# Performance work log

Measured on AMD Instinct MI355X. Metric: run time of the kernel, lower is better.

The kernel has to match this reference:

```python
import jax, jax.numpy as jnp
import numpy as np

N_GRAPHS = 256      # graphs in the batch
N_PER = 52          # nodes per peptide graph (module default num_nodes=52)
IN_CH = 21          # amino-acid one-hot features
HIDDEN = 128
OUT_EG = 128
LATENT = 64
N_LAYERS = 4


def _fc_edges(n_graphs, n_per):
    """Block-diagonal fully-connected directed edges (no self loops)."""
    base = np.arange(n_per)
    r, c = np.meshgrid(base, base, indexing='ij')
    mask = r != c
    r, c = r[mask], c[mask]                       # [n_per*(n_per-1)]
    offs = (np.arange(n_graphs) * n_per)[:, None]
    row = (r[None, :] + offs).reshape(-1)
    col = (c[None, :] + offs).reshape(-1)
    return row.astype(np.int32), col.astype(np.int32)


def setup_inputs() -> dict:
    key = jax.random.key(0)
    ks = iter(jax.random.split(key, 40))

    def rn(shape, scale=0.05):
        return jax.random.normal(next(ks), shape, dtype=jnp.float32) * scale

    N = N_GRAPHS * N_PER
    row, col = _fc_edges(N_GRAPHS, N_PER)
    L, H = N_LAYERS, HIDDEN
    return {
        'x': jax.random.normal(next(ks), (N, IN_CH), dtype=jnp.float32),
        'pos': jax.random.normal(next(ks), (N, 3), dtype=jnp.float32),
        'edge_row': jnp.asarray(row),
        'edge_col': jnp.asarray(col),
        'batch': jnp.repeat(jnp.arange(N_GRAPHS, dtype=jnp.int32), N_PER),
        'emb_in_w': rn((IN_CH, H)), 'emb_in_b': jnp.zeros((H,), jnp.float32),
        'edge_w1': rn((L, 2 * H + 1, H)), 'edge_b1': jnp.zeros((L, H), jnp.float32),
        'edge_w2': rn((L, H, H)), 'edge_b2': jnp.zeros((L, H), jnp.float32),
        'node_w1': rn((L, 2 * H, H)), 'node_b1': jnp.zeros((L, H), jnp.float32),
        'node_w2': rn((L, H, H)), 'node_b2': jnp.zeros((L, H), jnp.float32),
        'coord_w1': rn((L, H, H)), 'coord_b1': jnp.zeros((L, H), jnp.float32),
        'coord_w2': rn((L, H, 1), scale=0.001),   # xavier gain=0.001, no bias
        'emb_out_w': rn((H, OUT_EG)), 'emb_out_b': jnp.zeros((OUT_EG,), jnp.float32),
        'mean_w': rn((OUT_EG, LATENT)), 'mean_b': jnp.zeros((LATENT,), jnp.float32),
        'logvar_w': rn((OUT_EG, LATENT)), 'logvar_b': jnp.zeros((LATENT,), jnp.float32),
    }


def _segment_mean(data, ids, n):
    s = jax.ops.segment_sum(data, ids, num_segments=n)
    cnt = jax.ops.segment_sum(jnp.ones((data.shape[0],), data.dtype), ids, num_segments=n)
    return s / jnp.clip(cnt, 1.0)[:, None]


def _egcl(h, coord, row, col, p):
    """One E_GCL layer (residual=True, coords_agg='mean', no attention/tanh/normalize)."""
    ew1, eb1, ew2, eb2, nw1, nb1, nw2, nb2, cw1, cb1, cw2 = p
    n = h.shape[0]
    coord_diff = coord[row] - coord[col]                     # [E,3]
    radial = jnp.sum(coord_diff * coord_diff, axis=1, keepdims=True)  # [E,1]
    # edge model
    m = jnp.concatenate([h[row], h[col], radial], axis=1)    # [E,2H+1]
    m = jax.nn.silu(m @ ew1 + eb1)
    edge_feat = jax.nn.silu(m @ ew2 + eb2)                   # [E,H]
    # coord model: per-edge scalar, mean-aggregated onto source nodes
    t = jax.nn.silu(edge_feat @ cw1 + cb1) @ cw2             # [E,1]
    coord = coord + _segment_mean(coord_diff * t, row, n)
    # node model: sum-aggregate edge features, MLP, residual
    agg = jax.ops.segment_sum(edge_feat, row, num_segments=n)
    z = jnp.concatenate([h, agg], axis=1)                    # [N,2H]
    z = jax.nn.silu(z @ nw1 + nb1)
    h = h + (z @ nw2 + nb2)
    return h, coord


def reference(x, pos, edge_row, edge_col, batch,
              emb_in_w, emb_in_b,
              edge_w1, edge_b1, edge_w2, edge_b2,
              node_w1, node_b1, node_w2, node_b2,
              coord_w1, coord_b1, coord_w2,
              emb_out_w, emb_out_b,
              mean_w, mean_b, logvar_w, logvar_b):
    h = x @ emb_in_w + emb_in_b
    coord = pos
    for i in range(edge_w1.shape[0]):
        h, coord = _egcl(h, coord, edge_row, edge_col,
                         (edge_w1[i], edge_b1[i], edge_w2[i], edge_b2[i],
                          node_w1[i], node_b1[i], node_w2[i], node_b2[i],
                          coord_w1[i], coord_b1[i], coord_w2[i]))
    h = h @ emb_out_w + emb_out_b                            # embedding_out
    g = _segment_mean(h, batch, N_GRAPHS)                    # global_mean_pool
    mean = g @ mean_w + mean_b
    log_var = g @ logvar_w + logvar_b
    return mean, log_var
```

## Files before the change

kernel.cpp:

```cpp
#include <hip/hip_runtime.h>

constexpr int NPER = 52;
constexpr int HID  = 128;
constexpr int INCH = 21;
constexpr int NLAY = 4;
constexpr int LATD = 64;
constexpr int NGRAPH = 256;
constexpr int TPB  = 1024;

typedef short short8 __attribute__((ext_vector_type(8)));
typedef float f32x4  __attribute__((ext_vector_type(4)));

constexpr int W1T_OFF = 0;
constexpr int W1T_SZ  = NLAY * 256 * HID;
constexpr int W2T_OFF = W1T_OFF + W1T_SZ;
constexpr int W2T_SZ  = NLAY * HID * HID;
constexpr int C1T_OFF = W2T_OFF + W2T_SZ;
constexpr int C1T_SZ  = NLAY * HID * HID;
constexpr int N1T_OFF = C1T_OFF + C1T_SZ;
constexpr int N1T_SZ  = NLAY * HID * 2 * HID;
constexpr int N2T_OFF = N1T_OFF + N1T_SZ;
constexpr int N2T_SZ  = NLAY * HID * HID;
constexpr int WS_ELEMS = N2T_OFF + N2T_SZ;

__device__ __forceinline__ unsigned cvt_pk_bf16(float a, float b) {
    unsigned r;
    asm("v_cvt_pk_bf16_f32 %0, %1, %2" : "=v"(r) : "v"(a), "v"(b));
    return r;
}
__device__ __forceinline__ unsigned short f2bf(float f) {
    return (unsigned short)cvt_pk_bf16(f, f);
}
__device__ __forceinline__ float bf2f(unsigned short h) {
    return __uint_as_float(((unsigned)h) << 16);
}
__device__ __forceinline__ float fast_rcp(float x) {
    float r;
    asm("v_rcp_f32 %0, %1" : "=v"(r) : "v"(x));
    return r;
}
__device__ __forceinline__ float silu_f(float v) {
    return v * fast_rcp(1.0f + __expf(-v));
}

__device__ __forceinline__ f32x4 mfma16(short8 a, short8 b, f32x4 c) {
    return __builtin_amdgcn_mfma_f32_16x16x32_bf16(a, b, c, 0, 0, 0);
}

__device__ __forceinline__ int swz(int row, int e) {
    return row * HID + (e ^ ((row & 7) << 3));
}
__device__ __forceinline__ short8 ldA(const unsigned short* base, int row, int e) {
    return *(const short8*)(base + swz(row, e));
}

__global__ void conv_w(const float* __restrict__ ew1, const float* __restrict__ ew2,
                       const float* __restrict__ cw1, const float* __restrict__ nw1,
                       const float* __restrict__ nw2, unsigned short* __restrict__ ws)
{
    int idx = blockIdx.x * 256 + threadIdx.x;
    if (idx >= WS_ELEMS) return;
    float v;
    if (idx < W2T_OFF) {
        int t = idx - W1T_OFF;
        int L = t / (256 * HID), rem = t % (256 * HID);
        int n = rem / HID, k = rem % HID;
        v = (n < HID) ? ew1[(size_t)L * 257 * HID + k * HID + n]
                      : ew1[(size_t)L * 257 * HID + (HID + k) * HID + (n - HID)];
    } else if (idx < C1T_OFF) {
        int t = idx - W2T_OFF;
        int L = t / (HID * HID), rem = t % (HID * HID);
        int n = rem / HID, k = rem % HID;
        v = ew2[(size_t)L * HID * HID + k * HID + n];
    } else if (idx < N1T_OFF) {
        int t = idx - C1T_OFF;
        int L = t / (HID * HID), rem = t % (HID * HID);
        int n = rem / HID, k = rem % HID;
        v = cw1[(size_t)L * HID * HID + k * HID + n];
    } else if (idx < N2T_OFF) {
        int t = idx - N1T_OFF;
        int L = t / (HID * 2 * HID), rem = t % (HID * 2 * HID);
        int n = rem / (2 * HID), k = rem % (2 * HID);
        v = nw1[(size_t)L * 2 * HID * HID + k * HID + n];
    } else {
        int t = idx - N2T_OFF;
        int L = t / (HID * HID), rem = t % (HID * HID);
        int n = rem / HID, k = rem % HID;
        v = nw2[(size_t)L * HID * HID + k * HID + n];
    }
    ws[idx] = f2bf(v);
}

constexpr int LDS_SHORTS = 6 * NPER * HID;
constexpr int LDS_FLOATS = 4 * HID + NPER * 3 + NPER * 3 + 64 + 256 + HID;
constexpr size_t SHMEM_BYTES = LDS_SHORTS * 2 + LDS_FLOATS * 4;

extern "C" __global__ void __launch_bounds__(TPB)
egnn_mfma(const float* __restrict__ x, const float* __restrict__ pos,
          const float* __restrict__ emb_in_w, const float* __restrict__ emb_in_b,
          const float* __restrict__ edge_w1,
          const float* __restrict__ edge_b1, const float* __restrict__ edge_b2,
          const float* __restrict__ node_b1, const float* __restrict__ node_b2,
          const float* __restrict__ coord_b1, const float* __restrict__ coord_w2,
          const float* __restrict__ emb_out_w, const float* __restrict__ emb_out_b,
          const float* __restrict__ mean_w, const float* __restrict__ mean_b,
          const float* __restrict__ logvar_w, const float* __restrict__ logvar_b,
          const unsigned short* __restrict__ ws, float* __restrict__ out)
{
    extern __shared__ char smem[];
    unsigned short* m_s  = (unsigned short*)smem;
    unsigned short* ef_s = m_s  + NPER * HID;
    unsigned short* h_s  = ef_s + NPER * HID;
    unsigned short* ag_s = h_s  + NPER * HID;
    unsigned short* A_s  = ag_s + NPER * HID;
    unsigned short* B_s  = A_s  + NPER * HID;
    float* aggp    = (float*)(B_s + NPER * HID);
    float* coord_s = aggp + 4 * HID;
    float* cacc_s  = coord_s + NPER * 3;
    float* rad_s   = cacc_s + NPER * 3;
    float* tpart   = rad_s + 64;
    float* wr_s    = tpart + 256;

    const int g    = blockIdx.x;
    const int tid  = threadIdx.x;
    const int lane = tid & 63;
    const int wv   = tid >> 6;
    const int mt   = wv & 3;
    const int nq   = wv >> 2;
    const int l15  = lane & 15;
    const int kb   = lane >> 4;
    const int rowA = mt * 16 + l15;
    const int crow0 = mt * 16 + kb * 4;
    const int n0   = l15 + 16 * (2 * nq);
    const int n1   = n0 + 16;

    {
        float* xs = (float*)m_s;
        for (int p = tid; p < NPER * INCH; p += TPB) xs[p] = x[(size_t)g * NPER * INCH + p];
        for (int p = tid; p < NPER * 3; p += TPB)    coord_s[p] = pos[(size_t)g * NPER * 3 + p];
    }
    __syncthreads();

    for (int p = tid; p < NPER * HID; p += TPB) {
        int c = p >> 7, j = p & 127;
        float s = emb_in_b[j];
        #pragma unroll 7
        for (int k = 0; k < INCH; ++k) s += ((float*)m_s)[c * INCH + k] * emb_in_w[k * HID + j];
        h_s[swz(c, j)] = f2bf(s);
    }
    __syncthreads();

    for (int L = 0; L < NLAY; ++L) {
        const unsigned short* w1t = ws + W1T_OFF + (size_t)L * 256 * HID;
        const unsigned short* w2t = ws + W2T_OFF + (size_t)L * HID * HID;
        const unsigned short* c1t = ws + C1T_OFF + (size_t)L * HID * HID;
        const unsigned short* n1t = ws + N1T_OFF + (size_t)L * HID * 2 * HID;
        const unsigned short* n2t = ws + N2T_OFF + (size_t)L * HID * HID;

        short8 wE[8], wC[8];
        #pragma unroll
        for (int s = 0; s < 4; ++s) {
            wE[s]     = *(const short8*)(w2t + (size_t)n0 * HID + 32 * s + 8 * kb);
            wE[4 + s] = *(const short8*)(w2t + (size_t)n1 * HID + 32 * s + 8 * kb);
            wC[s]     = *(const short8*)(c1t + (size_t)n0 * HID + 32 * s + 8 * kb);
            wC[4 + s] = *(const short8*)(c1t + (size_t)n1 * HID + 32 * s + 8 * kb);
        }
        float eb2v[2], cb1v[2], cw2v[2];
        eb2v[0] = edge_b2[L * HID + n0];  eb2v[1] = edge_b2[L * HID + n1];
        cb1v[0] = coord_b1[L * HID + n0]; cb1v[1] = coord_b1[L * HID + n1];
        cw2v[0] = coord_w2[L * HID + n0]; cw2v[1] = coord_w2[L * HID + n1];
        if (tid < HID) wr_s[tid] = edge_w1[(size_t)L * 257 * HID + 256 * HID + tid];

        {
            f32x4 acc[4];
            #pragma unroll
            for (int q = 0; q < 4; ++q) acc[q] = (f32x4){0.f, 0.f, 0.f, 0.f};
            #pragma unroll
            for (int s = 0; s < 4; ++s) {
                short8 af = ldA(h_s, rowA, 32 * s + 8 * kb);
                #pragma unroll
                for (int q = 0; q < 4; ++q) {
                    int n = l15 + 16 * (4 * nq + q);
                    short8 bf = *(const short8*)(w1t + (size_t)n * HID + 32 * s + 8 * kb);
                    acc[q] = mfma16(af, bf, acc[q]);
                }
            }
            #pragma unroll
            for (int q = 0; q < 4; ++q) {
                int n = l15 + 16 * (4 * nq + q);
                float eb1 = (n < HID) ? edge_b1[L * HID + n] : 0.f;
                #pragma unroll
                for (int reg = 0; reg < 4; ++reg) {
                    int c = crow0 + reg;
                    if (c < NPER) {
                        float v = acc[q][reg] + eb1;
                        if (n < HID) A_s[swz(c, n)] = f2bf(v);
                        else         B_s[swz(c, n - HID)] = f2bf(v);
                    }
                }
            }
        }
        if (tid < NPER) {
            float dx = coord_s[0] - coord_s[tid * 3 + 0];
            float dy = coord_s[1] - coord_s[tid * 3 + 1];
            float dz = coord_s[2] - coord_s[tid * 3 + 2];
            rad_s[tid] = dx * dx + dy * dy + dz * dz;
        }
        __syncthreads();

        for (int r = 0; r < NPER; ++r) {
            if (wv == 0) {
                if (r > 0) {
                    const int rp = r - 1;
                    float dx = 0.f, dy = 0.f, dz = 0.f;
                    if (lane < NPER) {
                        float tc = tpart[lane] + tpart[64 + lane] + tpart[128 + lane] + tpart[192 + lane];
                        dx = (coord_s[rp * 3 + 0] - coord_s[lane * 3 + 0]) * tc;
                        dy = (coord_s[rp * 3 + 1] - coord_s[lane * 3 + 1]) * tc;
                        dz = (coord_s[rp * 3 + 2] - coord_s[lane * 3 + 2]) * tc;
                    }
                    #pragma unroll
                    for (int msk = 1; msk < 64; msk <<= 1) {
                        dx += __shfl_xor(dx, msk);
                        dy += __shfl_xor(dy, msk);
                        dz += __shfl_xor(dz, msk);
                    }
                    if (lane == 0) {
                        cacc_s[rp * 3 + 0] = dx; cacc_s[rp * 3 + 1] = dy; cacc_s[rp * 3 + 2] = dz;
                    }
                }
            } else {
                for (int p = tid - 64; p < NPER * 64; p += TPB - 64) {
                    int c = p >> 6, jp = (p & 63) * 2;
                    unsigned aA = *(const unsigned*)(A_s + swz(r, jp));
                    unsigned aB = *(const unsigned*)(B_s + swz(c, jp));
                    float rad = rad_s[c];
                    float2 w2v = *(const float2*)(wr_s + jp);
                    float v0 = bf2f((unsigned short)(aA & 0xffff)) + bf2f((unsigned short)(aB & 0xffff)) + rad * w2v.x;
                    float v1 = bf2f((unsigned short)(aA >> 16))    + bf2f((unsigned short)(aB >> 16))    + rad * w2v.y;
                    *(unsigned*)(m_s + swz(c, jp)) = cvt_pk_bf16(silu_f(v0), silu_f(v1));
                }
            }
            __syncthreads();

            {
                f32x4 e0 = (f32x4){0.f,0.f,0.f,0.f}, e1 = (f32x4){0.f,0.f,0.f,0.f};
                #pragma unroll
                for (int s = 0; s < 4; ++s) {
                    short8 af = ldA(m_s, rowA, 32 * s + 8 * kb);
                    e0 = mfma16(af, wE[s], e0);
                    e1 = mfma16(af, wE[4 + s], e1);
                }
                float asum0 = 0.f, asum1 = 0.f;
                #pragma unroll
                for (int reg = 0; reg < 4; ++reg) {
                    int c = crow0 + reg;
                    bool ok = (c < NPER) && (c != r);
                    float v0 = silu_f(e0[reg] + eb2v[0]);
                    float v1 = silu_f(e1[reg] + eb2v[1]);
                    if (c < NPER) {
                        ef_s[swz(c, n0)] = f2bf(v0);
                        ef_s[swz(c, n1)] = f2bf(v1);
                    }
                    if (ok) { asum0 += v0; asum1 += v1; }
                }
                asum0 += __shfl_xor(asum0, 16); asum0 += __shfl_xor(asum0, 32);
                asum1 += __shfl_xor(asum1, 16); asum1 += __shfl_xor(asum1, 32);
                if (kb == 0) {
                    aggp[mt * HID + n0] = asum0;
                    aggp[mt * HID + n1] = asum1;
                }
            }
            __syncthreads();

            {
                f32x4 y0 = (f32x4){0.f,0.f,0.f,0.f}, y1 = (f32x4){0.f,0.f,0.f,0.f};
                #pragma unroll
                for (int s = 0; s < 4; ++s) {
                    short8 af = ldA(ef_s, rowA, 32 * s + 8 * kb);
                    y0 = mfma16(af, wC[s], y0);
                    y1 = mfma16(af, wC[4 + s], y1);
                }
                #pragma unroll
                for (int reg = 0; reg < 4; ++reg) {
                    float v = silu_f(y0[reg] + cb1v[0]) * cw2v[0]
                            + silu_f(y1[reg] + cb1v[1]) * cw2v[1];
                    v += __shfl_xor(v, 1); v += __shfl_xor(v, 2);
                    v += __shfl_xor(v, 4); v += __shfl_xor(v, 8);
                    if (l15 == 0) tpart[nq * 64 + crow0 + reg] = v;
                }
            }
            if (tid < HID) {
                float a = aggp[tid] + aggp[HID + tid] + aggp[2 * HID + tid] + aggp[3 * HID + tid];
                ag_s[swz(r, tid)] = f2bf(a);
            }
            {
                int t2 = tid - 128;
                if (t2 >= 0 && t2 < NPER && r + 1 < NPER) {
                    int rn = r + 1;
                    float dx = coord_s[rn * 3 + 0] - coord_s[t2 * 3 + 0];
                    float dy = coord_s[rn * 3 + 1] - coord_s[t2 * 3 + 1];
                    float dz = coord_s[rn * 3 + 2] - coord_s[t2 * 3 + 2];
                    rad_s[t2] = dx * dx + dy * dy + dz * dz;
                }
            }
            __syncthreads();
        }

        if (wv == 0) {
            const int rp = NPER - 1;
            float dx = 0.f, dy = 0.f, dz = 0.f;
            if (lane < NPER) {
                float tc = tpart[lane] + tpart[64 + lane] + tpart[128 + lane] + tpart[192 + lane];
                dx = (coord_s[rp * 3 + 0] - coord_s[lane * 3 + 0]) * tc;
                dy = (coord_s[rp * 3 + 1] - coord_s[lane * 3 + 1]) * tc;
                dz = (coord_s[rp * 3 + 2] - coord_s[lane * 3 + 2]) * tc;
            }
            #pragma unroll
            for (int msk = 1; msk < 64; msk <<= 1) {
                dx += __shfl_xor(dx, msk);
                dy += __shfl_xor(dy, msk);
                dz += __shfl_xor(dz, msk);
            }
            if (lane == 0) {
                cacc_s[rp * 3 + 0] = dx; cacc_s[rp * 3 + 1] = dy; cacc_s[rp * 3 + 2] = dz;
            }
        }
        __syncthreads();

        if (tid < NPER * 3) coord_s[tid] += cacc_s[tid] * (1.0f / 51.0f);

        {
            float nb1v[2];
            nb1v[0] = node_b1[L * HID + n0]; nb1v[1] = node_b1[L * HID + n1];
            f32x4 z0 = (f32x4){0.f,0.f,0.f,0.f}, z1 = (f32x4){0.f,0.f,0.f,0.f};
            #pragma unroll
            for (int s = 0; s < 4; ++s) {
                short8 af = ldA(h_s, rowA, 32 * s + 8 * kb);
                z0 = mfma16(af, *(const short8*)(n1t + (size_t)n0 * 2 * HID + 32 * s + 8 * kb), z0);
                z1 = mfma16(af, *(const short8*)(n1t + (size_t)n1 * 2 * HID + 32 * s + 8 * kb), z1);
            }
            #pragma unroll
            for (int s = 0; s < 4; ++s) {
                short8 af = ldA(ag_s, rowA, 32 * s + 8 * kb);
                z0 = mfma16(af, *(const short8*)(n1t + (size_t)n0 * 2 * HID + HID + 32 * s + 8 * kb), z0);
                z1 = mfma16(af, *(const short8*)(n1t + (size_t)n1 * 2 * HID + HID + 32 * s + 8 * kb), z1);
            }
            #pragma unroll
            for (int reg = 0; reg < 4; ++reg) {
                int c = crow0 + reg;
                if (c < NPER) {
                    m_s[swz(c, n0)] = f2bf(silu_f(z0[reg] + nb1v[0]));
                    m_s[swz(c, n1)] = f2bf(silu_f(z1[reg] + nb1v[1]));
                }
            }
        }
        __syncthreads();

        {
            float nb2v[2];
            nb2v[0] = node_b2[L * HID + n0]; nb2v[1] = node_b2[L * HID + n1];
            f32x4 d0 = (f32x4){0.f,0.f,0.f,0.f}, d1 = (f32x4){0.f,0.f,0.f,0.f};
            #pragma unroll
            for (int s = 0; s < 4; ++s) {
                short8 af = ldA(m_s, rowA, 32 * s + 8 * kb);
                d0 = mfma16(af, *(const short8*)(n2t + (size_t)n0 * HID + 32 * s + 8 * kb), d0);
                d1 = mfma16(af, *(const short8*)(n2t + (size_t)n1 * HID + 32 * s + 8 * kb), d1);
            }
            #pragma unroll
            for (int reg = 0; reg < 4; ++reg) {
                int c = crow0 + reg;
                if (c < NPER) {
                    int i0 = swz(c, n0), i1 = swz(c, n1);
                    h_s[i0] = f2bf(bf2f(h_s[i0]) + d0[reg] + nb2v[0]);
                    h_s[i1] = f2bf(bf2f(h_s[i1]) + d1[reg] + nb2v[1]);
                }
            }
        }
        __syncthreads();
    }

    float* gm = aggp;
    float* eg = aggp + HID;
    if (tid < HID) {
        float s = 0.f;
        for (int c = 0; c < NPER; ++c) s += bf2f(h_s[swz(c, tid)]);
        gm[tid] = s * (1.0f / 52.0f);
    }
    __syncthreads();
    if (tid < HID) {
        float s = emb_out_b[tid];
        #pragma unroll 4
        for (int k = 0; k < HID; ++k) s += gm[k] * emb_out_w[k * HID + tid];
        eg[tid] = s;
    }
    __syncthreads();
    if (tid < 2 * LATD) {
        const int  l   = tid & (LATD - 1);
        const bool ism = tid < LATD;
        const float* W = ism ? mean_w : logvar_w;
        float s = ism ? mean_b[l] : logvar_b[l];
        #pragma unroll 4
        for (int k = 0; k < HID; ++k) s += eg[k] * W[k * LATD + l];
        out[(ism ? 0 : NGRAPH * LATD) + g * LATD + l] = s;
    }
}

extern "C" void kernel_launch(void* const* d_in, const int* in_sizes, int n_in,
                              void* d_out, int out_size, void* d_ws, size_t ws_size,
                              hipStream_t stream) {
    const float* x         = (const float*)d_in[0];
    const float* pos       = (const float*)d_in[1];
    const float* emb_in_w  = (const float*)d_in[5];
    const float* emb_in_b  = (const float*)d_in[6];
    const float* edge_w1   = (const float*)d_in[7];
    const float* edge_b1   = (const float*)d_in[8];
    const float* edge_w2   = (const float*)d_in[9];
    const float* edge_b2   = (const float*)d_in[10];
    const float* node_w1   = (const float*)d_in[11];
    const float* node_b1   = (const float*)d_in[12];
    const float* node_w2   = (const float*)d_in[13];
    const float* node_b2   = (const float*)d_in[14];
    const float* coord_w1  = (const float*)d_in[15];
    const float* coord_b1  = (const float*)d_in[16];
    const float* coord_w2  = (const float*)d_in[17];
    const float* emb_out_w = (const float*)d_in[18];
    const float* emb_out_b = (const float*)d_in[19];
    const float* mean_w    = (const float*)d_in[20];
    const float* mean_b    = (const float*)d_in[21];
    const float* logvar_w  = (const float*)d_in[22];
    const float* logvar_b  = (const float*)d_in[23];

    unsigned short* ws = (unsigned short*)d_ws;

    conv_w<<<(WS_ELEMS + 255) / 256, 256, 0, stream>>>(edge_w1, edge_w2, coord_w1,
                                                       node_w1, node_w2, ws);

    (void)hipFuncSetAttribute(reinterpret_cast<const void*>(egnn_mfma),
                              hipFuncAttributeMaxDynamicSharedMemorySize,
                              (int)SHMEM_BYTES);

    hipLaunchKernelGGL(egnn_mfma, dim3(NGRAPH), dim3(TPB), SHMEM_BYTES, stream,
                       x, pos, emb_in_w, emb_in_b, edge_w1,
                       edge_b1, edge_b2, node_b1, node_b2,
                       coord_b1, coord_w2, emb_out_w, emb_out_b,
                       mean_w, mean_b, logvar_w, logvar_b,
                       ws, (float*)d_out);
}
```

Baseline: 863.7 us.

## Process two receiver rows per edge-loop iteration with tiled LDS layout

The per-receiver edge loop now handles two receiver rows per iteration, which halves the number of barrier-separated phases per layer and gives each wave twice as many MFMAs per phase. The activation buffers move from an XOR-swizzled row layout to a padded k-chunked tile layout (stride 424) so fragment loads become simple offsets. The coordinate aggregation is folded into the pipeline of the next pair, and all waves now join the message-construction phase. In exchange the kernel uses more LDS (extra m/e buffers) and more registers, and the padded tile may cause different bank-conflict behaviour.

```diff
diff --git a/kernel.cpp b/kernel.cpp
--- a/kernel.cpp
+++ b/kernel.cpp
@@ -7,6 +7,8 @@
 constexpr int LATD = 64;
 constexpr int NGRAPH = 256;
 constexpr int TPB  = 1024;
+constexpr int TSTR = 424;
+constexpr int TILE = 16 * TSTR;
 
 typedef short short8 __attribute__((ext_vector_type(8)));
 typedef float f32x4  __attribute__((ext_vector_type(4)));
@@ -42,16 +44,12 @@
 __device__ __forceinline__ float silu_f(float v) {
     return v * fast_rcp(1.0f + __expf(-v));
 }
-
 __device__ __forceinline__ f32x4 mfma16(short8 a, short8 b, f32x4 c) {
     return __builtin_amdgcn_mfma_f32_16x16x32_bf16(a, b, c, 0, 0, 0);
 }
 
-__device__ __forceinline__ int swz(int row, int e) {
-    return row * HID + (e ^ ((row & 7) << 3));
-}
-__device__ __forceinline__ short8 ldA(const unsigned short* base, int row, int e) {
-    return *(const short8*)(base + swz(row, e));
+__device__ __forceinline__ int tidx(int row, int e) {
+    return (e >> 3) * TSTR + row * 8 + (e & 7);
 }
 
 __global__ void conv_w(const float* __restrict__ ew1, const float* __restrict__ ew2,
@@ -91,9 +89,28 @@
     ws[idx] = f2bf(v);
 }
 
-constexpr int LDS_SHORTS = 6 * NPER * HID;
-constexpr int LDS_FLOATS = 4 * HID + NPER * 3 + NPER * 3 + 64 + 256 + HID;
-constexpr size_t SHMEM_BYTES = LDS_SHORTS * 2 + LDS_FLOATS * 4;
+constexpr int LDS_FLOATS = 1024 + 156 + 156 + 128 + 512 + 128;
+constexpr size_t SHMEM_BYTES = (size_t)8 * TILE * 2 + LDS_FLOATS * 4;
+
+__device__ __forceinline__ void coord_agg(int r, int rr, const float* tpart,
+                                          const float* coord_s, float* cacc_s, int lane)
+{
+    float dx = 0.f, dy = 0.f, dz = 0.f;
+    if (lane < NPER) {
+        const float* tb = tpart + rr * 256;
+        float tc = tb[lane] + tb[64 + lane] + tb[128 + lane] + tb[192 + lane];
+        dx = (coord_s[r * 3 + 0] - coord_s[lane * 3 + 0]) * tc;
+        dy = (coord_s[r * 3 + 1] - coord_s[lane * 3 + 1]) * tc;
+        dz = (coord_s[r * 3 + 2] - coord_s[lane * 3 + 2]) * tc;
+    }
+    #pragma unroll
+    for (int m = 1; m < 64; m <<= 1) {
+        dx += __shfl_xor(dx, m); dy += __shfl_xor(dy, m); dz += __shfl_xor(dz, m);
+    }
+    if (lane == 0) {
+        cacc_s[r * 3 + 0] = dx; cacc_s[r * 3 + 1] = dy; cacc_s[r * 3 + 2] = dz;
+    }
+}
 
 extern "C" __global__ void __launch_bounds__(TPB)
 egnn_mfma(const float* __restrict__ x, const float* __restrict__ pos,
@@ -107,35 +124,40 @@
           const float* __restrict__ logvar_w, const float* __restrict__ logvar_b,
           const unsigned short* __restrict__ ws, float* __restrict__ out)
 {
-    extern __shared__ char smem[];
-    unsigned short* m_s  = (unsigned short*)smem;
-    unsigned short* ef_s = m_s  + NPER * HID;
-    unsigned short* h_s  = ef_s + NPER * HID;
-    unsigned short* ag_s = h_s  + NPER * HID;
-    unsigned short* A_s  = ag_s + NPER * HID;
-    unsigned short* B_s  = A_s  + NPER * HID;
-    float* aggp    = (float*)(B_s + NPER * HID);
-    float* coord_s = aggp + 4 * HID;
-    float* cacc_s  = coord_s + NPER * 3;
-    float* rad_s   = cacc_s + NPER * 3;
-    float* tpart   = rad_s + 64;
-    float* wr_s    = tpart + 256;
+    extern __shared__ __align__(16) char smem[];
+    unsigned short* m0_t = (unsigned short*)smem;
+    unsigned short* m1_t = m0_t + TILE;
+    unsigned short* e0_t = m1_t + TILE;
+    unsigned short* e1_t = e0_t + TILE;
+    unsigned short* h_t  = e1_t + TILE;
+    unsigned short* ag_t = h_t  + TILE;
+    unsigned short* A_t  = ag_t + TILE;
+    unsigned short* B_t  = A_t  + TILE;
+    float* aggp    = (float*)(B_t + TILE);
+    float* coord_s = aggp + 1024;
+    float* cacc_s  = coord_s + 156;
+    float* rad_s   = cacc_s + 156;
+    float* tpart   = rad_s + 128;
+    float* wr_s    = tpart + 512;
 
     const int g    = blockIdx.x;
     const int tid  = threadIdx.x;
     const int lane = tid & 63;
     const int wv   = tid >> 6;
-    const int mt   = wv & 3;
-    const int nq   = wv >> 2;
+    const int mp   = wv >> 2;
+    const int np   = wv & 3;
     const int l15  = lane & 15;
     const int kb   = lane >> 4;
-    const int rowA = mt * 16 + l15;
-    const int crow0 = mt * 16 + kb * 4;
-    const int n0   = l15 + 16 * (2 * nq);
+    const int rowA = mp * 16 + l15;
+    const int crow0 = mp * 16 + kb * 4;
+    const int n0   = 32 * np + l15;
     const int n1   = n0 + 16;
+    const int jp   = 2 * lane;
+    const int pb   = (jp >> 3) * TSTR + (jp & 7);
+    const int fo   = kb * TSTR + rowA * 8;
 
     {
-        float* xs = (float*)m_s;
+        float* xs = (float*)m0_t;
         for (int p = tid; p < NPER * INCH; p += TPB) xs[p] = x[(size_t)g * NPER * INCH + p];
         for (int p = tid; p < NPER * 3; p += TPB)    coord_s[p] = pos[(size_t)g * NPER * 3 + p];
     }
@@ -145,8 +167,8 @@
         int c = p >> 7, j = p & 127;
         float s = emb_in_b[j];
         #pragma unroll 7
-        for (int k = 0; k < INCH; ++k) s += ((float*)m_s)[c * INCH + k] * emb_in_w[k * HID + j];
-        h_s[swz(c, j)] = f2bf(s);
+        for (int k = 0; k < INCH; ++k) s += ((float*)m0_t)[c * INCH + k] * emb_in_w[k * HID + j];
+        h_t[tidx(c, j)] = f2bf(s);
     }
     __syncthreads();
 
@@ -177,25 +199,25 @@
             for (int q = 0; q < 4; ++q) acc[q] = (f32x4){0.f, 0.f, 0.f, 0.f};
             #pragma unroll
             for (int s = 0; s < 4; ++s) {
-                short8 af = ldA(h_s, rowA, 32 * s + 8 * kb);
+                short8 af = *(const short8*)(h_t + fo + s * 4 * TSTR);
                 #pragma unroll
                 for (int q = 0; q < 4; ++q) {
-                    int n = l15 + 16 * (4 * nq + q);
+                    int n = l15 + 16 * (4 * np + q);
                     short8 bf = *(const short8*)(w1t + (size_t)n * HID + 32 * s + 8 * kb);
                     acc[q] = mfma16(af, bf, acc[q]);
                 }
             }
             #pragma unroll
             for (int q = 0; q < 4; ++q) {
-                int n = l15 + 16 * (4 * nq + q);
+                int n = l15 + 16 * (4 * np + q);
                 float eb1 = (n < HID) ? edge_b1[L * HID + n] : 0.f;
                 #pragma unroll
                 for (int reg = 0; reg < 4; ++reg) {
                     int c = crow0 + reg;
                     if (c < NPER) {
                         float v = acc[q][reg] + eb1;
-                        if (n < HID) A_s[swz(c, n)] = f2bf(v);
-                        else         B_s[swz(c, n - HID)] = f2bf(v);
+                        if (n < HID) A_t[tidx(c, n)] = f2bf(v);
+                        else         B_t[tidx(c, n - HID)] = f2bf(v);
                     }
                 }
             }
@@ -205,144 +227,131 @@
             float dy = coord_s[1] - coord_s[tid * 3 + 1];
             float dz = coord_s[2] - coord_s[tid * 3 + 2];
             rad_s[tid] = dx * dx + dy * dy + dz * dz;
+        } else if (tid >= 64 && tid < 64 + NPER) {
+            int c = tid - 64;
+            float dx = coord_s[3] - coord_s[c * 3 + 0];
+            float dy = coord_s[4] - coord_s[c * 3 + 1];
+            float dz = coord_s[5] - coord_s[c * 3 + 2];
+            rad_s[64 + c] = dx * dx + dy * dy + dz * dz;
         }
         __syncthreads();
 
-        for (int r = 0; r < NPER; ++r) {
-            if (wv == 0) {
-                if (r > 0) {
-                    const int rp = r - 1;
-                    float dx = 0.f, dy = 0.f, dz = 0.f;
-                    if (lane < NPER) {
-                        float tc = tpart[lane] + tpart[64 + lane] + tpart[128 + lane] + tpart[192 + lane];
-                        dx = (coord_s[rp * 3 + 0] - coord_s[lane * 3 + 0]) * tc;
-                        dy = (coord_s[rp * 3 + 1] - coord_s[lane * 3 + 1]) * tc;
-                        dz = (coord_s[rp * 3 + 2] - coord_s[lane * 3 + 2]) * tc;
+        const float wrl = wr_s[jp], wrh = wr_s[jp + 1];
+
+        for (int gp = 0; gp < 26; ++gp) {
+            const int r0 = 2 * gp, r1 = r0 + 1;
+
+            {
+                unsigned pa0 = *(const unsigned*)(A_t + pb + r0 * 8);
+                unsigned pa1 = *(const unsigned*)(A_t + pb + r1 * 8);
+                float A0l = bf2f((unsigned short)(pa0 & 0xffff)), A0h = bf2f((unsigned short)(pa0 >> 16));
+                float A1l = bf2f((unsigned short)(pa1 & 0xffff)), A1h = bf2f((unsigned short)(pa1 >> 16));
+                for (int j = wv; j < 2 * NPER; j += 16) {
+                    int rr = (j >= NPER);
+                    int c  = rr ? j - NPER : j;
+                    float Al = rr ? A1l : A0l, Ah = rr ? A1h : A0h;
+                    float rad = rad_s[rr * 64 + c];
+                    unsigned bp = *(const unsigned*)(B_t + pb + c * 8);
+                    float v0 = Al + bf2f((unsigned short)(bp & 0xffff)) + rad * wrl;
+                    float v1 = Ah + bf2f((unsigned short)(bp >> 16))    + rad * wrh;
+                    unsigned mv = cvt_pk_bf16(silu_f(v0), silu_f(v1));
+                    *(unsigned*)((rr ? m1_t : m0_t) + pb + c * 8) = mv;
+                }
+            }
+            __syncthreads();
+
+            {
+                f32x4 e00 = (f32x4){0.f,0.f,0.f,0.f}, e01 = e00, e10 = e00, e11 = e00;
+                #pragma unroll
+                for (int s = 0; s < 4; ++s) {
+                    short8 af0 = *(const short8*)(m0_t + fo + s * 4 * TSTR);
+                    short8 af1 = *(const short8*)(m1_t + fo + s * 4 * TSTR);
+                    e00 = mfma16(af0, wE[s], e00); e01 = mfma16(af0, wE[4 + s], e01);
+                    e10 = mfma16(af1, wE[s], e10); e11 = mfma16(af1, wE[4 + s], e11);
+                }
+                #pragma unroll
+                for (int rr = 0; rr < 2; ++rr) {
+                    f32x4 ea = rr ? e10 : e00, eb = rr ? e11 : e01;
+                    unsigned short* et = rr ? e1_t : e0_t;
+                    const int r = rr ? r1 : r0;
+                    float a0 = 0.f, a1 = 0.f;
+                    #pragma unroll
+                    for (int reg = 0; reg < 4; ++reg) {
+                        int c = crow0 + reg;
+                        float v0 = silu_f(ea[reg] + eb2v[0]);
+                        float v1 = silu_f(eb[reg] + eb2v[1]);
+                        if (c < NPER) {
+                            et[tidx(c, n0)] = f2bf(v0);
+                            et[tidx(c, n1)] = f2bf(v1);
+                            if (c != r) { a0 += v0; a1 += v1; }
+                        }
                     }
+                    a0 += __shfl_xor(a0, 16); a0 += __shfl_xor(a0, 32);
+                    a1 += __shfl_xor(a1, 16); a1 += __shfl_xor(a1, 32);
+                    if (kb == 0) {
+                        float* ar = aggp + (rr * 4 + mp) * HID;
+                        ar[n0] = a0; ar[n1] = a1;
+                    }
+                }
+                if (wv < 2 && gp > 0) coord_agg(2 * gp - 2 + wv, wv, tpart, coord_s, cacc_s, lane);
+            }
+            __syncthreads();
+
+            {
+                f32x4 y00 = (f32x4){0.f,0.f,0.f,0.f}, y01 = y00, y10 = y00, y11 = y00;
+                #pragma unroll
+                for (int s = 0; s < 4; ++s) {
+                    short8 af0 = *(const short8*)(e0_t + fo + s * 4 * TSTR);
+                    short8 af1 = *(const short8*)(e1_t + fo + s * 4 * TSTR);
+                    y00 = mfma16(af0, wC[s], y00); y01 = mfma16(af0, wC[4 + s], y01);
+                    y10 = mfma16(af1, wC[s], y10); y11 = mfma16(af1, wC[4 + s], y11);
+                }
+                #pragma unroll
+                for (int rr = 0; rr < 2; ++rr) {
+                    f32x4 ya = rr ? y10 : y00, yb = rr ? y11 : y01;
+                    float* tp = tpart + (rr * 4 + np) * 64;
                     #pragma unroll
-                    for (int msk = 1; msk < 64; msk <<= 1) {
-                        dx += __shfl_xor(dx, msk);
-                        dy += __shfl_xor(dy, msk);
-                        dz += __shfl_xor(dz, msk);
+                    for (int reg = 0; reg < 4; ++reg) {
+                        float v = silu_f(ya[reg] + cb1v[0]) * cw2v[0]
+                                + silu_f(yb[reg] + cb1v[1]) * cw2v[1];
+                        v += __shfl_xor(v, 1); v += __shfl_xor(v, 2);
+                        v += __shfl_xor(v, 4); v += __shfl_xor(v, 8);
+                        if (l15 == 0) tp[crow0 + reg] = v;
                     }
-                    if (lane == 0) {
-                        cacc_s[rp * 3 + 0] = dx; cacc_s[rp * 3 + 1] = dy; cacc_s[rp * 3 + 2] = dz;
-                    }
-                }
-            } else {
-                for (int p = tid - 64; p < NPER * 64; p += TPB - 64) {
-                    int c = p >> 6, jp = (p & 63) * 2;
-                    unsigned aA = *(const unsigned*)(A_s + swz(r, jp));
-                    unsigned aB = *(const unsigned*)(B_s + swz(c, jp));
-                    float rad = rad_s[c];
-                    float2 w2v = *(const float2*)(wr_s + jp);
-                    float v0 = bf2f((unsigned short)(aA & 0xffff)) + bf2f((unsigned short)(aB & 0xffff)) + rad * w2v.x;
-                    float v1 = bf2f((unsigned short)(aA >> 16))    + bf2f((unsigned short)(aB >> 16))    + rad * w2v.y;
-                    *(unsigned*)(m_s + swz(c, jp)) = cvt_pk_bf16(silu_f(v0), silu_f(v1));
+                }
+            }
+            if (tid < 256) {
+                int rr = tid >> 7, t = tid & 127;
+                const float* ap = aggp + rr * 512;
+                float a = ap[t] + ap[128 + t] + ap[256 + t] + ap[384 + t];
+                ag_t[tidx(2 * gp + rr, t)] = f2bf(a);
+            } else if (tid < 384 && gp + 1 < 26) {
+                int t = tid - 256, rr = t >> 6, c = t & 63;
+                if (c < NPER) {
+                    int r = 2 * (gp + 1) + rr;
+                    float dx = coord_s[r * 3 + 0] - coord_s[c * 3 + 0];
+                    float dy = coord_s[r * 3 + 1] - coord_s[c * 3 + 1];
+                    float dz = coord_s[r * 3 + 2] - coord_s[c * 3 + 2];
+                    rad_s[rr * 64 + c] = dx * dx + dy * dy + dz * dz;
                 }
             }
             __syncthreads();
-
-            {
-                f32x4 e0 = (f32x4){0.f,0.f,0.f,0.f}, e1 = (f32x4){0.f,0.f,0.f,0.f};
-                #pragma unroll
-                for (int s = 0; s < 4; ++s) {
-                    short8 af = ldA(m_s, rowA, 32 * s + 8 * kb);
-                    e0 = mfma16(af, wE[s], e0);
-                    e1 = mfma16(af, wE[4 + s], e1);
-                }
-                float asum0 = 0.f, asum1 = 0.f;
-                #pragma unroll
-                for (int reg = 0; reg < 4; ++reg) {
-                    int c = crow0 + reg;
-                    bool ok = (c < NPER) && (c != r);
-                    float v0 = silu_f(e0[reg] + eb2v[0]);
-                    float v1 = silu_f(e1[reg] + eb2v[1]);
-                    if (c < NPER) {
-                        ef_s[swz(c, n0)] = f2bf(v0);
-                        ef_s[swz(c, n1)] = f2bf(v1);
-                    }
-                    if (ok) { asum0 += v0; asum1 += v1; }
-                }
-                asum0 += __shfl_xor(asum0, 16); asum0 += __shfl_xor(asum0, 32);
-                asum1 += __shfl_xor(asum1, 16); asum1 += __shfl_xor(asum1, 32);
-                if (kb == 0) {
-                    aggp[mt * HID + n0] = asum0;
-                    aggp[mt * HID + n1] = asum1;
-                }
-            }
-            __syncthreads();
-
-            {
-                f32x4 y0 = (f32x4){0.f,0.f,0.f,0.f}, y1 = (f32x4){0.f,0.f,0.f,0.f};
-                #pragma unroll
-                for (int s = 0; s < 4; ++s) {
-                    short8 af = ldA(ef_s, rowA, 32 * s + 8 * kb);
-                    y0 = mfma16(af, wC[s], y0);
-                    y1 = mfma16(af, wC[4 + s], y1);
-                }
-                #pragma unroll
-                for (int reg = 0; reg < 4; ++reg) {
-                    float v = silu_f(y0[reg] + cb1v[0]) * cw2v[0]
-                            + silu_f(y1[reg] + cb1v[1]) * cw2v[1];
-                    v += __shfl_xor(v, 1); v += __shfl_xor(v, 2);
-                    v += __shfl_xor(v, 4); v += __shfl_xor(v, 8);
-                    if (l15 == 0) tpart[nq * 64 + crow0 + reg] = v;
-                }
-            }
-            if (tid < HID) {
-                float a = aggp[tid] + aggp[HID + tid] + aggp[2 * HID + tid] + aggp[3 * HID + tid];
-                ag_s[swz(r, tid)] = f2bf(a);
-            }
-            {
-                int t2 = tid - 128;
-                if (t2 >= 0 && t2 < NPER && r + 1 < NPER) {
-                    int rn = r + 1;
-                    float dx = coord_s[rn * 3 + 0] - coord_s[t2 * 3 + 0];
-                    float dy = coord_s[rn * 3 + 1] - coord_s[t2 * 3 + 1];
-                    float dz = coord_s[rn * 3 + 2] - coord_s[t2 * 3 + 2];
-                    rad_s[t2] = dx * dx + dy * dy + dz * dz;
-                }
-            }
-            __syncthreads();
-        }
-
-        if (wv == 0) {
-            const int rp = NPER - 1;
-            float dx = 0.f, dy = 0.f, dz = 0.f;
-            if (lane < NPER) {
-                float tc = tpart[lane] + tpart[64 + lane] + tpart[128 + lane] + tpart[192 + lane];
-                dx = (coord_s[rp * 3 + 0] - coord_s[lane * 3 + 0]) * tc;
-                dy = (coord_s[rp * 3 + 1] - coord_s[lane * 3 + 1]) * tc;
-                dz = (coord_s[rp * 3 + 2] - coord_s[lane * 3 + 2]) * tc;
-            }
-            #pragma unroll
-            for (int msk = 1; msk < 64; msk <<= 1) {
-                dx += __shfl_xor(dx, msk);
-                dy += __shfl_xor(dy, msk);
-                dz += __shfl_xor(dz, msk);
-            }
-            if (lane == 0) {
-                cacc_s[rp * 3 + 0] = dx; cacc_s[rp * 3 + 1] = dy; cacc_s[rp * 3 + 2] = dz;
-            }
-        }
-        __syncthreads();
-
-        if (tid < NPER * 3) coord_s[tid] += cacc_s[tid] * (1.0f / 51.0f);
-
+        }
+
+        if (wv < 2) coord_agg(50 + wv, wv, tpart, coord_s, cacc_s, lane);
         {
             float nb1v[2];
             nb1v[0] = node_b1[L * HID + n0]; nb1v[1] = node_b1[L * HID + n1];
-            f32x4 z0 = (f32x4){0.f,0.f,0.f,0.f}, z1 = (f32x4){0.f,0.f,0.f,0.f};
+            f32x4 z0 = (f32x4){0.f,0.f,0.f,0.f}, z1 = z0;
             #pragma unroll
             for (int s = 0; s < 4; ++s) {
-                short8 af = ldA(h_s, rowA, 32 * s + 8 * kb);
+                short8 af = *(const short8*)(h_t + fo + s * 4 * TSTR);
                 z0 = mfma16(af, *(const short8*)(n1t + (size_t)n0 * 2 * HID + 32 * s + 8 * kb), z0);
                 z1 = mfma16(af, *(const short8*)(n1t + (size_t)n1 * 2 * HID + 32 * s + 8 * kb), z1);
             }
             #pragma unroll
             for (int s = 0; s < 4; ++s) {
-                short8 af = ldA(ag_s, rowA, 32 * s + 8 * kb);
+                short8 af = *(const short8*)(ag_t + fo + s * 4 * TSTR);
                 z0 = mfma16(af, *(const short8*)(n1t + (size_t)n0 * 2 * HID + HID + 32 * s + 8 * kb), z0);
                 z1 = mfma16(af, *(const short8*)(n1t + (size_t)n1 * 2 * HID + HID + 32 * s + 8 * kb), z1);
             }
@@ -350,20 +359,21 @@
             for (int reg = 0; reg < 4; ++reg) {
                 int c = crow0 + reg;
                 if (c < NPER) {
-                    m_s[swz(c, n0)] = f2bf(silu_f(z0[reg] + nb1v[0]));
-                    m_s[swz(c, n1)] = f2bf(silu_f(z1[reg] + nb1v[1]));
+                    m0_t[tidx(c, n0)] = f2bf(silu_f(z0[reg] + nb1v[0]));
+                    m0_t[tidx(c, n1)] = f2bf(silu_f(z1[reg] + nb1v[1]));
                 }
             }
         }
         __syncthreads();
 
+        if (tid < NPER * 3) coord_s[tid] += cacc_s[tid] * (1.0f / 51.0f);
         {
             float nb2v[2];
             nb2v[0] = node_b2[L * HID + n0]; nb2v[1] = node_b2[L * HID + n1];
-            f32x4 d0 = (f32x4){0.f,0.f,0.f,0.f}, d1 = (f32x4){0.f,0.f,0.f,0.f};
+            f32x4 d0 = (f32x4){0.f,0.f,0.f,0.f}, d1 = d0;
             #pragma unroll
             for (int s = 0; s < 4; ++s) {
-                short8 af = ldA(m_s, rowA, 32 * s + 8 * kb);
+                short8 af = *(const short8*)(m0_t + fo + s * 4 * TSTR);
                 d0 = mfma16(af, *(const short8*)(n2t + (size_t)n0 * HID + 32 * s + 8 * kb), d0);
                 d1 = mfma16(af, *(const short8*)(n2t + (size_t)n1 * HID + 32 * s + 8 * kb), d1);
             }
@@ -371,9 +381,9 @@
             for (int reg = 0; reg < 4; ++reg) {
                 int c = crow0 + reg;
                 if (c < NPER) {
-                    int i0 = swz(c, n0), i1 = swz(c, n1);
-                    h_s[i0] = f2bf(bf2f(h_s[i0]) + d0[reg] + nb2v[0]);
-                    h_s[i1] = f2bf(bf2f(h_s[i1]) + d1[reg] + nb2v[1]);
+                    int i0 = tidx(c, n0), i1 = tidx(c, n1);
+                    h_t[i0] = f2bf(bf2f(h_t[i0]) + d0[reg] + nb2v[0]);
+                    h_t[i1] = f2bf(bf2f(h_t[i1]) + d1[reg] + nb2v[1]);
                 }
             }
         }
@@ -384,7 +394,7 @@
     float* eg = aggp + HID;
     if (tid < HID) {
         float s = 0.f;
-        for (int c = 0; c < NPER; ++c) s += bf2f(h_s[swz(c, tid)]);
+        for (int c = 0; c < NPER; ++c) s += bf2f(h_t[tidx(c, tid)]);
         gm[tid] = s * (1.0f / 52.0f);
     }
     __syncthreads();
```

After: 805.7 us. 6.7% less time.
